# Performance work log

Hardware: AMD Instinct MI355X
Metric: run time of the kernel (lower is better)

Reference implementation:

```python
import jax, jax.numpy as jnp
import numpy as np
import math

B, L, D, H = 2, 2048, 1024, 16

def setup_inputs() -> dict:
    key = jax.random.key(0)
    ks = jax.random.split(key, 5)
    return {
        "query": jax.random.normal(ks[0], (B, L, D), dtype=jnp.float32),
        "key": jax.random.normal(ks[1], (B, L, D), dtype=jnp.float32),
        "value": jax.random.normal(ks[2], (B, L, D), dtype=jnp.float32),
        "w_out": jax.random.normal(ks[3], (D, D), dtype=jnp.float32) * (1.0 / math.sqrt(D)),
        "b_out": jnp.zeros((D,), dtype=jnp.float32),
    }

def reference(query, key, value, w_out, b_out):
    b, l, d_model = query.shape
    num_heads = H
    head_dim = d_model // num_heads
    scaling = 1.0 / math.sqrt(d_model)  # NOTE: module scales by embed_dim, not head_dim

    def reshape(x):
        return x.reshape(b, l, num_heads, head_dim).transpose(0, 2, 1, 3)  # [B,H,L,hd]

    q, k, v = reshape(query), reshape(key), reshape(value)
    scores = jnp.einsum("bhqd,bhkd->bhqk", q, k) * scaling  # [B,H,L,L]

    u = max(1, int(math.ceil(math.log(l + 1))))  # static: 8 for L=2048
    _, topk_idx = jax.lax.top_k(scores, u)  # [B,H,L,u]

    # scatter True at top-u key positions per query
    bi = jnp.arange(b)[:, None, None, None]
    hi = jnp.arange(num_heads)[None, :, None, None]
    qi = jnp.arange(l)[None, None, :, None]
    mask = jnp.zeros(scores.shape, dtype=bool).at[bi, hi, qi, topk_idx].set(True)

    scores_masked = jnp.where(mask, scores, -jnp.inf)
    attn_weights = jax.nn.softmax(scores_masked, axis=-1)  # [B,H,L,L]

    attn_out = jnp.einsum("bhqk,bhkd->bhqd", attn_weights, v)
    attn_out = attn_out.transpose(0, 2, 1, 3).reshape(b, l, d_model)
    attn_out = attn_out @ w_out.T + b_out  # nn.Linear
    return attn_out, attn_weights
```

## Files before the change

### kernel.cpp

```cpp
#include <hip/hip_runtime.h>
#include <math.h>

#define BB 2
#define LL 2048
#define DD 1024
#define HH 16
#define SCALE 0.03125f

#define ATTN_ELEMS ((size_t)BB * LL * DD)

typedef unsigned short u16;
typedef __attribute__((ext_vector_type(8))) short bf16x8;
typedef __attribute__((ext_vector_type(4))) short s16x4;
typedef __attribute__((ext_vector_type(4))) float f32x4;

__device__ __forceinline__ u16 f2bf_rne(float f) {
    union { float f; unsigned u; } c; c.f = f;
    unsigned u = c.u;
    u += 0x7fffu + ((u >> 16) & 1u);
    return (u16)(u >> 16);
}

__device__ __forceinline__ void splitbf(float x, short& h, short& l) {
    union { float f; unsigned u; } c; c.f = x;
    unsigned uh = c.u & 0xFFFF0000u;
    h = (short)(uh >> 16);
    union { unsigned u; float f; } ch; ch.u = uh;
    l = (short)f2bf_rne(x - ch.f);
}

__device__ __forceinline__ void insert8(float (&tv)[8], int (&ti)[8], float cv, int ci) {
    bool g0 = cv > tv[0], g1 = cv > tv[1], g2 = cv > tv[2], g3 = cv > tv[3],
         g4 = cv > tv[4], g5 = cv > tv[5], g6 = cv > tv[6];
    tv[7] = g6 ? tv[6] : cv;                 ti[7] = g6 ? ti[6] : ci;
    tv[6] = g5 ? tv[5] : (g6 ? cv : tv[6]);  ti[6] = g5 ? ti[5] : (g6 ? ci : ti[6]);
    tv[5] = g4 ? tv[4] : (g5 ? cv : tv[5]);  ti[5] = g4 ? ti[4] : (g5 ? ci : ti[5]);
    tv[4] = g3 ? tv[3] : (g4 ? cv : tv[4]);  ti[4] = g3 ? ti[3] : (g4 ? ci : ti[4]);
    tv[3] = g2 ? tv[2] : (g3 ? cv : tv[3]);  ti[3] = g2 ? ti[2] : (g3 ? ci : ti[3]);
    tv[2] = g1 ? tv[1] : (g2 ? cv : tv[2]);  ti[2] = g1 ? ti[1] : (g2 ? ci : ti[2]);
    tv[1] = g0 ? tv[0] : (g1 ? cv : tv[1]);  ti[1] = g0 ? ti[0] : (g1 ? ci : ti[1]);
    tv[0] = g0 ? cv : tv[0];                 ti[0] = g0 ? ci : ti[0];
}

__device__ __forceinline__ void insert12(float (&tv)[12], int (&ti)[12], float cv, int ci) {
    bool g0 = cv > tv[0], g1 = cv > tv[1], g2 = cv > tv[2], g3 = cv > tv[3],
         g4 = cv > tv[4], g5 = cv > tv[5], g6 = cv > tv[6], g7 = cv > tv[7],
         g8 = cv > tv[8], g9 = cv > tv[9], g10 = cv > tv[10];
    tv[11] = g10 ? tv[10] : cv;                 ti[11] = g10 ? ti[10] : ci;
    tv[10] = g9 ? tv[9] : (g10 ? cv : tv[10]);  ti[10] = g9 ? ti[9] : (g10 ? ci : ti[10]);
    tv[9]  = g8 ? tv[8] : (g9 ? cv : tv[9]);    ti[9]  = g8 ? ti[8] : (g9 ? ci : ti[9]);
    tv[8]  = g7 ? tv[7] : (g8 ? cv : tv[8]);    ti[8]  = g7 ? ti[7] : (g8 ? ci : ti[8]);
    tv[7]  = g6 ? tv[6] : (g7 ? cv : tv[7]);    ti[7]  = g6 ? ti[6] : (g7 ? ci : ti[7]);
    tv[6]  = g5 ? tv[5] : (g6 ? cv : tv[6]);    ti[6]  = g5 ? ti[5] : (g6 ? ci : ti[6]);
    tv[5]  = g4 ? tv[4] : (g5 ? cv : tv[5]);    ti[5]  = g4 ? ti[4] : (g5 ? ci : ti[5]);
    tv[4]  = g3 ? tv[3] : (g4 ? cv : tv[4]);    ti[4]  = g3 ? ti[3] : (g4 ? ci : ti[4]);
    tv[3]  = g2 ? tv[2] : (g3 ? cv : tv[3]);    ti[3]  = g2 ? ti[2] : (g3 ? ci : ti[3]);
    tv[2]  = g1 ? tv[1] : (g2 ? cv : tv[2]);    ti[2]  = g1 ? ti[1] : (g2 ? ci : ti[2]);
    tv[1]  = g0 ? tv[0] : (g1 ? cv : tv[1]);    ti[1]  = g0 ? ti[0] : (g1 ? ci : ti[1]);
    tv[0]  = g0 ? cv : tv[0];                   ti[0]  = g0 ? ci : ti[0];
}

__device__ __forceinline__ void merge4(
    const float* v0, const int* i0, const float* v1, const int* i1,
    const float* v2, const int* i2, const float* v3, const int* i3,
    float* ov, int* oi)
{
    int p0 = 0, p1 = 0, p2 = 0, p3 = 0;
    #pragma unroll
    for (int s = 0; s < 8; ++s) {
        float a0 = v0[p0], a1 = v1[p1], a2 = v2[p2], a3 = v3[p3];
        int   b0 = i0[p0], b1 = i1[p1], b2 = i2[p2], b3 = i3[p3];
        float bv = a0; int bi = b0; int bc = 0;
        if (a1 > bv || (a1 == bv && b1 < bi)) { bv = a1; bi = b1; bc = 1; }
        if (a2 > bv || (a2 == bv && b2 < bi)) { bv = a2; bi = b2; bc = 2; }
        if (a3 > bv || (a3 == bv && b3 < bi)) { bv = a3; bi = b3; bc = 3; }
        p0 += (bc == 0); p1 += (bc == 1); p2 += (bc == 2); p3 += (bc == 3);
        ov[s] = bv; oi[s] = bi;
    }
}


__global__ __launch_bounds__(256) void prep_k_kernel(
    const float* __restrict__ k, u16* __restrict__ khi, u16* __restrict__ klo)
{
    int gid = blockIdx.x * 256 + threadIdx.x;
    int li   = gid & 15;
    int qd   = (gid >> 4) & 3;
    int c    = (gid >> 6) & 1;
    int s    = (gid >> 7) & 127;
    int head = gid >> 14;
    int b = head >> 4, h = head & 15;
    const float* src = k + ((size_t)(b * LL + s * 16 + li)) * DD + h * 64 + c * 32 + qd * 8;
    float x[8];
    *(f32x4*)x       = *(const f32x4*)src;
    *(f32x4*)(x + 4) = *(const f32x4*)(src + 4);
    bf16x8 h8, l8;
    #pragma unroll
    for (int e = 0; e < 8; ++e) { short hh, ll; splitbf(x[e], hh, ll); h8[e] = hh; l8[e] = ll; }
    *(bf16x8*)&khi[(size_t)gid * 8] = h8;
    *(bf16x8*)&klo[(size_t)gid * 8] = l8;
}

__global__ __launch_bounds__(256) void prep_w_kernel(
    const float* __restrict__ w, u16* __restrict__ whi, u16* __restrict__ wlo)
{
    int gid = blockIdx.x * 256 + threadIdx.x;
    int li = gid & 15;
    int qd = (gid >> 4) & 3;
    int c  = (gid >> 6) & 3;
    int nt = (gid >> 8) & 3;
    int kc = (gid >> 10) & 7;
    int nb = gid >> 13;
    const float* src = w + (size_t)(nb * 64 + nt * 16 + li) * DD + kc * 128 + c * 32 + qd * 8;
    float x[8];
    *(f32x4*)x       = *(const f32x4*)src;
    *(f32x4*)(x + 4) = *(const f32x4*)(src + 4);
    bf16x8 h8, l8;
    #pragma unroll
    for (int e = 0; e < 8; ++e) { short hh, ll; splitbf(x[e], hh, ll); h8[e] = hh; l8[e] = ll; }
    *(bf16x8*)&whi[(size_t)gid * 8] = h8;
    *(bf16x8*)&wlo[(size_t)gid * 8] = l8;
}

__global__ __launch_bounds__(256) void attn_fast_kernel(
    const float* __restrict__ q, const float* __restrict__ k, const float* __restrict__ v,
    const u16* __restrict__ khi_g, const u16* __restrict__ klo_g,
    float* __restrict__ aw, u16* __restrict__ chi, u16* __restrict__ clo)
{
    const int swz  = (blockIdx.x & 7) * 128 + (blockIdx.x >> 3);
    const int qt   = swz & 31;
    const int h    = (swz >> 5) & 15;
    const int b    = swz >> 9;
    const int t    = threadIdx.x;
    const int wv   = t >> 6;
    const int lane = t & 63;
    const int li   = lane & 15;
    const int quad = lane >> 4;

    __shared__ float dv[64][48];
    __shared__ u16   di_s[64][48];
    __shared__ u16   cidx[64][12];

    f32x4* awz = (f32x4*)(aw + (((size_t)(b * HH + h) * LL) + (size_t)qt * 64) * LL);
    const f32x4 zero4 = {0.f, 0.f, 0.f, 0.f};

    bf16x8 qh0, ql0, qh1, ql1;
    {
        const float* qrow = q + ((size_t)(b * LL + qt * 64 + wv * 16 + li)) * DD + h * 64;
        float x[8];
        *(f32x4*)x       = *(const f32x4*)(qrow + quad * 8);
        *(f32x4*)(x + 4) = *(const f32x4*)(qrow + quad * 8 + 4);
        #pragma unroll
        for (int e = 0; e < 8; ++e) { short hh, ll; splitbf(x[e], hh, ll); qh0[e] = hh; ql0[e] = ll; }
        *(f32x4*)x       = *(const f32x4*)(qrow + 32 + quad * 8);
        *(f32x4*)(x + 4) = *(const f32x4*)(qrow + 32 + quad * 8 + 4);
        #pragma unroll
        for (int e = 0; e < 8; ++e) { short hh, ll; splitbf(x[e], hh, ll); qh1[e] = hh; ql1[e] = ll; }
    }

    float tv[12]; int tix[12];
    #pragma unroll
    for (int s = 0; s < 12; ++s) { tv[s] = -INFINITY; tix[s] = 0; }

    const u16* khb = khi_g + (size_t)(b * HH + h) * 131072 + (size_t)lane * 8;
    const u16* klb = klo_g + (size_t)(b * HH + h) * 131072 + (size_t)lane * 8;

    bf16x8 kh0 = *(const bf16x8*)(khb);
    bf16x8 kh1 = *(const bf16x8*)(khb + 512);
    bf16x8 kl0 = *(const bf16x8*)(klb);
    bf16x8 kl1 = *(const bf16x8*)(klb + 512);

    #pragma unroll 2
    for (int s = 0; s < 128; ++s) {
        const int sn = (s + 1) & 127;
        bf16x8 nh0 = *(const bf16x8*)(khb + (size_t)sn * 1024);
        bf16x8 nh1 = *(const bf16x8*)(khb + (size_t)sn * 1024 + 512);
        bf16x8 nl0 = *(const bf16x8*)(klb + (size_t)sn * 1024);
        bf16x8 nl1 = *(const bf16x8*)(klb + (size_t)sn * 1024 + 512);

        awz[s * 256 + t] = zero4;

        f32x4 c4a = {0.f, 0.f, 0.f, 0.f};
        f32x4 c4b = {0.f, 0.f, 0.f, 0.f};
        c4a = __builtin_amdgcn_mfma_f32_16x16x32_bf16(kh0, qh0, c4a, 0, 0, 0);
        c4b = __builtin_amdgcn_mfma_f32_16x16x32_bf16(kh1, qh1, c4b, 0, 0, 0);
        c4a = __builtin_amdgcn_mfma_f32_16x16x32_bf16(kl0, qh0, c4a, 0, 0, 0);
        c4b = __builtin_amdgcn_mfma_f32_16x16x32_bf16(kl1, qh1, c4b, 0, 0, 0);
        c4a = __builtin_amdgcn_mfma_f32_16x16x32_bf16(kh0, ql0, c4a, 0, 0, 0);
        c4b = __builtin_amdgcn_mfma_f32_16x16x32_bf16(kh1, ql1, c4b, 0, 0, 0);

        const int ci0 = s * 16 + quad * 4;
        #pragma unroll
        for (int r = 0; r < 4; ++r) {
            float cv = (c4a[r] + c4b[r]) * SCALE;
            if (cv > tv[11]) insert12(tv, tix, cv, ci0 + r);
        }
        kh0 = nh0; kh1 = nh1; kl0 = nl0; kl1 = nl1;
    }

    {
        const int row = wv * 16 + li;
        #pragma unroll
        for (int s = 0; s < 12; ++s) {
            dv[row][quad * 12 + s]   = tv[s];
            di_s[row][quad * 12 + s] = (u16)tix[s];
        }
    }
    __syncthreads();

    if (t < 64) {
        const float* v0 = &dv[t][0];   const u16* i0 = &di_s[t][0];
        const float* v1 = &dv[t][12];  const u16* i1 = &di_s[t][12];
        const float* v2 = &dv[t][24];  const u16* i2 = &di_s[t][24];
        const float* v3 = &dv[t][36];  const u16* i3 = &di_s[t][36];
        int p0 = 0, p1 = 0, p2 = 0, p3 = 0;
        #pragma unroll
        for (int s = 0; s < 12; ++s) {
            float a0 = v0[p0], a1 = v1[p1], a2 = v2[p2], a3 = v3[p3];
            int   b0 = i0[p0], b1 = i1[p1], b2 = i2[p2], b3 = i3[p3];
            float bv = a0; int bi = b0; int bc = 0;
            if (a1 > bv || (a1 == bv && b1 < bi)) { bv = a1; bi = b1; bc = 1; }
            if (a2 > bv || (a2 == bv && b2 < bi)) { bv = a2; bi = b2; bc = 2; }
            if (a3 > bv || (a3 == bv && b3 < bi)) { bv = a3; bi = b3; bc = 3; }
            p0 += (bc == 0); p1 += (bc == 1); p2 += (bc == 2); p3 += (bc == 3);
            cidx[t][s] = (u16)bi;
        }
    }
    __syncthreads();

    float* cs = &dv[0][0];
    for (int task = t; task < 768; task += 256) {
        int row = task / 12, c = task - row * 12;
        const float* qp = q + ((size_t)(b * LL + qt * 64 + row)) * DD + h * 64;
        const float* kp = k + ((size_t)(b * LL + (int)cidx[row][c])) * DD + h * 64;
        float acc = 0.f;
        for (int d4 = 0; d4 < 16; ++d4) {
            f32x4 qa = *(const f32x4*)(qp + d4 * 4);
            f32x4 ka = *(const f32x4*)(kp + d4 * 4);
            acc = fmaf(qa[0], ka[0], acc);
            acc = fmaf(qa[1], ka[1], acc);
            acc = fmaf(qa[2], ka[2], acc);
            acc = fmaf(qa[3], ka[3], acc);
        }
        cs[row * 12 + c] = acc * SCALE;
    }
    __syncthreads();

    float* wrow = &dv[0][0] + 1024;
    int*   wix  = (int*)&di_s[0][0];
    if (t < 64) {
        float vv[12]; int ii[12];
        #pragma unroll
        for (int c = 0; c < 12; ++c) { vv[c] = cs[t * 12 + c]; ii[c] = (int)cidx[t][c]; }
        float fv[8]; int fi[8];
        #pragma unroll
        for (int s = 0; s < 8; ++s) {
            float bv = -INFINITY; int bi = 0x7fffffff; int bc = 0;
            #pragma unroll
            for (int c = 0; c < 12; ++c) {
                if (vv[c] > bv || (vv[c] == bv && ii[c] < bi)) { bv = vv[c]; bi = ii[c]; bc = c; }
            }
            vv[bc] = -INFINITY;
            fv[s] = bv; fi[s] = bi;
        }
        float m = fv[0];
        float e0[8]; float sum = 0.f;
        #pragma unroll
        for (int s = 0; s < 8; ++s) { e0[s] = __expf(fv[s] - m); sum += e0[s]; }
        float inv = 1.0f / sum;
        float* awrow = aw + (((size_t)(b * HH + h) * LL) + (size_t)qt * 64 + t) * LL;
        #pragma unroll
        for (int s = 0; s < 8; ++s) {
            float w8 = e0[s] * inv;
            awrow[fi[s]] = w8;
            wrow[t * 8 + s] = w8; wix[t * 8 + s] = fi[s];
        }
    }
    __syncthreads();

    const float* vbase = v + ((size_t)b * LL) * DD + h * 64;
    #pragma unroll
    for (int i = 0; i < 4; ++i) {
        int id = i * 256 + t;
        int row = id >> 4, seg = id & 15;
        f32x4 acc = {0.f, 0.f, 0.f, 0.f};
        #pragma unroll
        for (int s = 0; s < 8; ++s) {
            float ws = wrow[row * 8 + s];
            f32x4 vvv = *(const f32x4*)(vbase + (size_t)wix[row * 8 + s] * DD + seg * 4);
            acc[0] = fmaf(ws, vvv[0], acc[0]);
            acc[1] = fmaf(ws, vvv[1], acc[1]);
            acc[2] = fmaf(ws, vvv[2], acc[2]);
            acc[3] = fmaf(ws, vvv[3], acc[3]);
        }
        size_t off = ((size_t)(b * LL + qt * 64 + row)) * DD + h * 64 + seg * 4;
        s16x4 h4, l4;
        #pragma unroll
        for (int j = 0; j < 4; ++j) { short hh, ll; splitbf(acc[j], hh, ll); h4[j] = hh; l4[j] = ll; }
        *(s16x4*)(chi + off) = h4;
        *(s16x4*)(clo + off) = l4;
    }
}

__global__ __launch_bounds__(256) void linear_fast_kernel(
    const u16* __restrict__ chi, const u16* __restrict__ clo,
    const u16* __restrict__ whi, const u16* __restrict__ wlo,
    const float* __restrict__ bias, float* __restrict__ out)
{
    const int bid  = blockIdx.x;
    const int nb   = bid & 15, mb = bid >> 4;
    const int t    = threadIdx.x;
    const int wv   = t >> 6;
    const int lane = t & 63;
    const int li   = lane & 15;
    const int quad = lane >> 4;

    f32x4 acc0 = {0.f,0.f,0.f,0.f}, acc1 = {0.f,0.f,0.f,0.f},
          acc2 = {0.f,0.f,0.f,0.f}, acc3 = {0.f,0.f,0.f,0.f};

    const u16* ah_row = chi + (size_t)(mb * 64 + wv * 16 + li) * DD + quad * 8;
    const u16* al_row = clo + (size_t)(mb * 64 + wv * 16 + li) * DD + quad * 8;
    const size_t wboff = (size_t)nb * 65536 + (size_t)lane * 8;

    for (int kc = 0; kc < 8; ++kc) {
        const u16* wb_h = whi + wboff + kc * 8192;
        const u16* wb_l = wlo + wboff + kc * 8192;
        #pragma unroll
        for (int c = 0; c < 4; ++c) {
            bf16x8 ah = *(const bf16x8*)(ah_row + kc * 128 + c * 32);
            bf16x8 al = *(const bf16x8*)(al_row + kc * 128 + c * 32);
            bf16x8 bh0 = *(const bf16x8*)(wb_h + c * 512);
            bf16x8 bl0 = *(const bf16x8*)(wb_l + c * 512);
            bf16x8 bh1 = *(const bf16x8*)(wb_h + 2048 + c * 512);
            bf16x8 bl1 = *(const bf16x8*)(wb_l + 2048 + c * 512);
            bf16x8 bh2 = *(const bf16x8*)(wb_h + 4096 + c * 512);
            bf16x8 bl2 = *(const bf16x8*)(wb_l + 4096 + c * 512);
            bf16x8 bh3 = *(const bf16x8*)(wb_h + 6144 + c * 512);
            bf16x8 bl3 = *(const bf16x8*)(wb_l + 6144 + c * 512);
            acc0 = __builtin_amdgcn_mfma_f32_16x16x32_bf16(ah, bh0, acc0, 0, 0, 0);
            acc0 = __builtin_amdgcn_mfma_f32_16x16x32_bf16(ah, bl0, acc0, 0, 0, 0);
            acc0 = __builtin_amdgcn_mfma_f32_16x16x32_bf16(al, bh0, acc0, 0, 0, 0);
            acc1 = __builtin_amdgcn_mfma_f32_16x16x32_bf16(ah, bh1, acc1, 0, 0, 0);
            acc1 = __builtin_amdgcn_mfma_f32_16x16x32_bf16(ah, bl1, acc1, 0, 0, 0);
            acc1 = __builtin_amdgcn_mfma_f32_16x16x32_bf16(al, bh1, acc1, 0, 0, 0);
            acc2 = __builtin_amdgcn_mfma_f32_16x16x32_bf16(ah, bh2, acc2, 0, 0, 0);
            acc2 = __builtin_amdgcn_mfma_f32_16x16x32_bf16(ah, bl2, acc2, 0, 0, 0);
            acc2 = __builtin_amdgcn_mfma_f32_16x16x32_bf16(al, bh2, acc2, 0, 0, 0);
            acc3 = __builtin_amdgcn_mfma_f32_16x16x32_bf16(ah, bh3, acc3, 0, 0, 0);
            acc3 = __builtin_amdgcn_mfma_f32_16x16x32_bf16(ah, bl3, acc3, 0, 0, 0);
            acc3 = __builtin_amdgcn_mfma_f32_16x16x32_bf16(al, bh3, acc3, 0, 0, 0);
        }
    }

    #pragma unroll
    for (int st = 0; st < 4; ++st) {
        f32x4 a = (st == 0) ? acc0 : (st == 1) ? acc1 : (st == 2) ? acc2 : acc3;
        int col = nb * 64 + st * 16 + li;
        float bb2 = bias[col];
        #pragma unroll
        for (int r = 0; r < 4; ++r)
            out[(size_t)(mb * 64 + wv * 16 + quad * 4 + r) * DD + col] = a[r] + bb2;
    }
}


__global__ __launch_bounds__(256) void attn_kernel(
    const float* __restrict__ q, const float* __restrict__ k, const float* __restrict__ v,
    float* __restrict__ aw, float* __restrict__ ctx)
{
    const int bid  = blockIdx.x;
    const int qt   = bid & 31;
    const int h    = (bid >> 5) & 15;
    const int b    = bid >> 9;
    const int t    = threadIdx.x;
    const int wv   = t >> 6;
    const int lane = t & 63;
    const int li   = lane & 15;
    const int quad = lane >> 4;

    __shared__ __align__(16) char smA[32768];
    __shared__ float s2v[32][4][8];
    __shared__ int   s2i[32][4][8];
    __shared__ int   cidx[32][12];
    __shared__ float cs[32][12];
    __shared__ float wrow[64][8];
    __shared__ int   wix[64][8];
    u16* khi = (u16*)smA;
    u16* klo = (u16*)(smA + 16384);

    const float* kbase = k + ((size_t)b * LL) * DD + h * 64;
    f32x4* awz = (f32x4*)(aw + (((size_t)(b * HH + h) * LL) + (size_t)qt * 64) * LL);
    const f32x4 zero4 = {0.f, 0.f, 0.f, 0.f};

    bf16x8 qh0, ql0, qh1, ql1;
    {
        const float* qrow = q + ((size_t)(b * LL + qt * 64 + wv * 16 + li)) * DD + h * 64;
        float x[8];
        *(f32x4*)x       = *(const f32x4*)(qrow + quad * 8);
        *(f32x4*)(x + 4) = *(const f32x4*)(qrow + quad * 8 + 4);
        #pragma unroll
        for (int e = 0; e < 8; ++e) { short hh, ll; splitbf(x[e], hh, ll); qh0[e] = hh; ql0[e] = ll; }
        *(f32x4*)x       = *(const f32x4*)(qrow + 32 + quad * 8);
        *(f32x4*)(x + 4) = *(const f32x4*)(qrow + 32 + quad * 8 + 4);
        #pragma unroll
        for (int e = 0; e < 8; ++e) { short hh, ll; splitbf(x[e], hh, ll); qh1[e] = hh; ql1[e] = ll; }
    }

    float tv[4][8]; int tix[4][8];
    #pragma unroll
    for (int r = 0; r < 4; ++r)
        #pragma unroll
        for (int s = 0; s < 8; ++s) { tv[r][s] = -INFINITY; tix[r][s] = 0; }

    for (int iter = 0; iter < 16; ++iter) {
        __syncthreads();
        #pragma unroll
        for (int j = 0; j < 4; ++j) {
            int f   = j * 256 + t;
            int col = f >> 3;
            int c   = (f >> 2) & 1;
            int qd  = f & 3;
            const float* src = kbase + (size_t)(iter * 128 + col) * DD + c * 32 + qd * 8;
            float x[8];
            *(f32x4*)x       = *(const f32x4*)src;
            *(f32x4*)(x + 4) = *(const f32x4*)(src + 4);
            bf16x8 h8, l8;
            #pragma unroll
            for (int e = 0; e < 8; ++e) { short hh, ll; splitbf(x[e], hh, ll); h8[e] = hh; l8[e] = ll; }
            int off = (((col >> 4) * 2 + c) << 9) + (qd << 7) + ((col & 15) << 3);
            *(bf16x8*)&khi[off] = h8;
            *(bf16x8*)&klo[off] = l8;
        }
        #pragma unroll
        for (int i = 0; i < 8; ++i) awz[iter * 2048 + i * 256 + t] = zero4;
        __syncthreads();

        #pragma unroll
        for (int s = 0; s < 8; ++s) {
            int fo = s << 10;
            bf16x8 kh0 = *(bf16x8*)&khi[fo + (lane << 3)];
            bf16x8 kh1 = *(bf16x8*)&khi[fo + 512 + (lane << 3)];
            bf16x8 kl0 = *(bf16x8*)&klo[fo + (lane << 3)];
            bf16x8 kl1 = *(bf16x8*)&klo[fo + 512 + (lane << 3)];
            f32x4 c4 = {0.f, 0.f, 0.f, 0.f};
            c4 = __builtin_amdgcn_mfma_f32_16x16x32_bf16(qh0, kh0, c4, 0, 0, 0);
            c4 = __builtin_amdgcn_mfma_f32_16x16x32_bf16(qh1, kh1, c4, 0, 0, 0);
            c4 = __builtin_amdgcn_mfma_f32_16x16x32_bf16(qh0, kl0, c4, 0, 0, 0);
            c4 = __builtin_amdgcn_mfma_f32_16x16x32_bf16(qh1, kl1, c4, 0, 0, 0);
            c4 = __builtin_amdgcn_mfma_f32_16x16x32_bf16(ql0, kh0, c4, 0, 0, 0);
            c4 = __builtin_amdgcn_mfma_f32_16x16x32_bf16(ql1, kh1, c4, 0, 0, 0);
            int ci = iter * 128 + s * 16 + li;
            #pragma unroll
            for (int r = 0; r < 4; ++r) {
                float cv = c4[r] * SCALE;
                if (cv > tv[r][7]) insert8(tv[r], tix[r], cv, ci);
            }
        }
    }

    float* mv = (float*)smA;
    int*   mi = (int*)(smA + 16384);
    for (int bb = 0; bb < 2; ++bb) {
        __syncthreads();
        if ((wv >> 1) == bb) {
            int rl0 = (wv & 1) * 16 + quad * 4;
            #pragma unroll
            for (int r = 0; r < 4; ++r) {
                int base = (rl0 + r) * 128 + li * 8;
                #pragma unroll
                for (int s = 0; s < 8; ++s) { mv[base + s] = tv[r][s]; mi[base + s] = tix[r][s]; }
            }
        }
        __syncthreads();
        if (t < 128) {
            int rr = t >> 2, p = t & 3;
            int base = rr * 128 + p * 32;
            merge4(&mv[base], &mi[base], &mv[base + 8], &mi[base + 8],
                   &mv[base + 16], &mi[base + 16], &mv[base + 24], &mi[base + 24],
                   s2v[rr][p], s2i[rr][p]);
        }
        __syncthreads();
        if (t < 32) {
            int rr = t;
            int pp[4] = {0, 0, 0, 0};
            #pragma unroll
            for (int s = 0; s < 12; ++s) {
                float bv = -INFINITY; int bi = 0x7fffffff; int bc = 0;
                #pragma unroll
                for (int l = 0; l < 4; ++l) {
                    if (pp[l] < 8) {
                        float hv = s2v[rr][l][pp[l]]; int hi2 = s2i[rr][l][pp[l]];
                        if (hv > bv || (hv == bv && hi2 < bi)) { bv = hv; bi = hi2; bc = l; }
                    }
                }
                pp[bc] += 1;
                cidx[rr][s] = bi;
            }
        }
        __syncthreads();
        for (int task = t; task < 384; task += 256) {
            int row = task / 12, c = task - row * 12;
            const float* qp = q + ((size_t)(b * LL + qt * 64 + bb * 32 + row)) * DD + h * 64;
            const float* kp = k + ((size_t)(b * LL + cidx[row][c])) * DD + h * 64;
            float acc = 0.f;
            for (int d4 = 0; d4 < 16; ++d4) {
                f32x4 qa = *(const f32x4*)(qp + d4 * 4);
                f32x4 ka = *(const f32x4*)(kp + d4 * 4);
                acc = fmaf(qa[0], ka[0], acc);
                acc = fmaf(qa[1], ka[1], acc);
                acc = fmaf(qa[2], ka[2], acc);
                acc = fmaf(qa[3], ka[3], acc);
            }
            cs[row][c] = acc * SCALE;
        }
        __syncthreads();
        if (t < 32) {
            int rr = t;
            float vv[12]; int ii[12];
            #pragma unroll
            for (int c = 0; c < 12; ++c) { vv[c] = cs[rr][c]; ii[c] = cidx[rr][c]; }
            float fv[8]; int fi[8];
            #pragma unroll
            for (int s = 0; s < 8; ++s) {
                float bv = -INFINITY; int bi = 0x7fffffff; int bc = 0;
                #pragma unroll
                for (int c = 0; c < 12; ++c) {
                    if (vv[c] > bv || (vv[c] == bv && ii[c] < bi)) { bv = vv[c]; bi = ii[c]; bc = c; }
                }
                vv[bc] = -INFINITY;
                fv[s] = bv; fi[s] = bi;
            }
            float m = fv[0];
            float e0[8]; float sum = 0.f;
            #pragma unroll
            for (int s = 0; s < 8; ++s) { e0[s] = __expf(fv[s] - m); sum += e0[s]; }
            float inv = 1.0f / sum;
            int grow = bb * 32 + rr;
            float* awrow = aw + (((size_t)(b * HH + h) * LL) + (size_t)qt * 64 + grow) * LL;
            #pragma unroll
            for (int s = 0; s < 8; ++s) {
                float w8 = e0[s] * inv;
                awrow[fi[s]] = w8;
                wrow[grow][s] = w8; wix[grow][s] = fi[s];
            }
        }
    }
    __syncthreads();

    const float* vbase = v + ((size_t)b * LL) * DD + h * 64;
    #pragma unroll
    for (int i = 0; i < 4; ++i) {
        int id = i * 256 + t;
        int row = id >> 4, seg = id & 15;
        f32x4 acc = {0.f, 0.f, 0.f, 0.f};
        #pragma unroll
        for (int s = 0; s < 8; ++s) {
            float ws = wrow[row][s];
            f32x4 vvv = *(const f32x4*)(vbase + (size_t)wix[row][s] * DD + seg * 4);
            acc[0] = fmaf(ws, vvv[0], acc[0]);
            acc[1] = fmaf(ws, vvv[1], acc[1]);
            acc[2] = fmaf(ws, vvv[2], acc[2]);
            acc[3] = fmaf(ws, vvv[3], acc[3]);
        }
        *(f32x4*)(ctx + ((size_t)(b * LL + qt * 64 + row)) * DD + h * 64 + seg * 4) = acc;
    }
}

__global__ __launch_bounds__(256) void linear_ws_kernel(
    const float* __restrict__ ctx, const float* __restrict__ w,
    const float* __restrict__ bias, float* __restrict__ out)
{
    const int bid  = blockIdx.x;
    const int nb   = bid & 15, mb = bid >> 4;
    const int t    = threadIdx.x;
    const int wv   = t >> 6;
    const int lane = t & 63;
    const int li   = lane & 15;
    const int quad = lane >> 4;

    __shared__ u16 bhi[8192], blo[8192];

    f32x4 acc0 = {0.f,0.f,0.f,0.f}, acc1 = {0.f,0.f,0.f,0.f},
          acc2 = {0.f,0.f,0.f,0.f}, acc3 = {0.f,0.f,0.f,0.f};
    const float* arow = ctx + (size_t)(mb * 64 + wv * 16 + li) * DD;

    for (int kc = 0; kc < 8; ++kc) {
        __syncthreads();
        #pragma unroll
        for (int j = 0; j < 4; ++j) {
            int f   = j * 256 + t;
            int col = f >> 4;
            int c   = (f >> 2) & 3;
            int qd  = f & 3;
            const float* src = w + (size_t)(nb * 64 + col) * DD + kc * 128 + c * 32 + qd * 8;
            float x[8];
            *(f32x4*)x       = *(const f32x4*)src;
            *(f32x4*)(x + 4) = *(const f32x4*)(src + 4);
            bf16x8 h8, l8;
            #pragma unroll
            for (int e = 0; e < 8; ++e) { short hh, ll; splitbf(x[e], hh, ll); h8[e] = hh; l8[e] = ll; }
            int off = (((col >> 4) * 4 + c) << 9) + (qd << 7) + ((col & 15) << 3);
            *(bf16x8*)&bhi[off] = h8;
            *(bf16x8*)&blo[off] = l8;
        }
        __syncthreads();

        bf16x8 ah[4], al[4];
        #pragma unroll
        for (int c = 0; c < 4; ++c) {
            float x[8];
            *(f32x4*)x       = *(const f32x4*)(arow + kc * 128 + c * 32 + quad * 8);
            *(f32x4*)(x + 4) = *(const f32x4*)(arow + kc * 128 + c * 32 + quad * 8 + 4);
            #pragma unroll
            for (int e = 0; e < 8; ++e) { short hh, ll; splitbf(x[e], hh, ll); ah[c][e] = hh; al[c][e] = ll; }
        }
        #pragma unroll
        for (int c = 0; c < 4; ++c) {
            bf16x8 bh0 = *(bf16x8*)&bhi[(( 0 + c) << 9) + (lane << 3)];
            bf16x8 bl0 = *(bf16x8*)&blo[(( 0 + c) << 9) + (lane << 3)];
            bf16x8 bh1 = *(bf16x8*)&bhi[(( 4 + c) << 9) + (lane << 3)];
            bf16x8 bl1 = *(bf16x8*)&blo[(( 4 + c) << 9) + (lane << 3)];
            bf16x8 bh2 = *(bf16x8*)&bhi[(( 8 + c) << 9) + (lane << 3)];
            bf16x8 bl2 = *(bf16x8*)&blo[(( 8 + c) << 9) + (lane << 3)];
            bf16x8 bh3 = *(bf16x8*)&bhi[((12 + c) << 9) + (lane << 3)];
            bf16x8 bl3 = *(bf16x8*)&blo[((12 + c) << 9) + (lane << 3)];
            acc0 = __builtin_amdgcn_mfma_f32_16x16x32_bf16(ah[c], bh0, acc0, 0, 0, 0);
            acc0 = __builtin_amdgcn_mfma_f32_16x16x32_bf16(ah[c], bl0, acc0, 0, 0, 0);
            acc0 = __builtin_amdgcn_mfma_f32_16x16x32_bf16(al[c], bh0, acc0, 0, 0, 0);
            acc1 = __builtin_amdgcn_mfma_f32_16x16x32_bf16(ah[c], bh1, acc1, 0, 0, 0);
            acc1 = __builtin_amdgcn_mfma_f32_16x16x32_bf16(ah[c], bl1, acc1, 0, 0, 0);
            acc1 = __builtin_amdgcn_mfma_f32_16x16x32_bf16(al[c], bh1, acc1, 0, 0, 0);
            acc2 = __builtin_amdgcn_mfma_f32_16x16x32_bf16(ah[c], bh2, acc2, 0, 0, 0);
            acc2 = __builtin_amdgcn_mfma_f32_16x16x32_bf16(ah[c], bl2, acc2, 0, 0, 0);
            acc2 = __builtin_amdgcn_mfma_f32_16x16x32_bf16(al[c], bh2, acc2, 0, 0, 0);
            acc3 = __builtin_amdgcn_mfma_f32_16x16x32_bf16(ah[c], bh3, acc3, 0, 0, 0);
            acc3 = __builtin_amdgcn_mfma_f32_16x16x32_bf16(ah[c], bl3, acc3, 0, 0, 0);
            acc3 = __builtin_amdgcn_mfma_f32_16x16x32_bf16(al[c], bh3, acc3, 0, 0, 0);
        }
    }

    #pragma unroll
    for (int st = 0; st < 4; ++st) {
        f32x4 a = (st == 0) ? acc0 : (st == 1) ? acc1 : (st == 2) ? acc2 : acc3;
        int col = nb * 64 + st * 16 + li;
        float bb2 = bias[col];
        #pragma unroll
        for (int r = 0; r < 4; ++r)
            out[(size_t)(mb * 64 + wv * 16 + quad * 4 + r) * DD + col] = a[r] + bb2;
    }
}

__global__ __launch_bounds__(256) void linear_inplace_kernel(
    float* io, const float* __restrict__ w, const float* __restrict__ bias)
{
    __shared__ u16 ahi[16384], alo[16384];
    const int t    = threadIdx.x;
    const int m0   = blockIdx.x * 16;
    const int wv   = t >> 6;
    const int lane = t & 63;
    const int li   = lane & 15;
    const int quad = lane >> 4;

    #pragma unroll
    for (int i = 0; i < 8; ++i) {
        int id  = i * 256 + t;
        int row = id >> 7;
        int c   = (id >> 2) & 31;
        int qd  = id & 3;
        const float* src = io + (size_t)(m0 + row) * DD + c * 32 + qd * 8;
        float x[8];
        *(f32x4*)x       = *(const f32x4*)src;
        *(f32x4*)(x + 4) = *(const f32x4*)(src + 4);
        bf16x8 h8, l8;
        #pragma unroll
        for (int e = 0; e < 8; ++e) { short hh, ll; splitbf(x[e], hh, ll); h8[e] = hh; l8[e] = ll; }
        int off = (c << 9) + (qd << 7) + (row << 3);
        *(bf16x8*)&ahi[off] = h8;
        *(bf16x8*)&alo[off] = l8;
    }
    __syncthreads();

    f32x4 acc[16];
    #pragma unroll
    for (int i = 0; i < 16; ++i) acc[i] = (f32x4){0.f, 0.f, 0.f, 0.f};

    for (int c = 0; c < 32; ++c) {
        bf16x8 ah = *(bf16x8*)&ahi[(c << 9) + (lane << 3)];
        bf16x8 al = *(bf16x8*)&alo[(c << 9) + (lane << 3)];
        #pragma unroll
        for (int sub = 0; sub < 16; ++sub) {
            int col = wv * 256 + sub * 16 + li;
            const float* src = w + (size_t)col * DD + c * 32 + quad * 8;
            float x[8];
            *(f32x4*)x       = *(const f32x4*)src;
            *(f32x4*)(x + 4) = *(const f32x4*)(src + 4);
            bf16x8 bh, bl;
            #pragma unroll
            for (int e = 0; e < 8; ++e) { short hh, ll; splitbf(x[e], hh, ll); bh[e] = hh; bl[e] = ll; }
            acc[sub] = __builtin_amdgcn_mfma_f32_16x16x32_bf16(ah, bh, acc[sub], 0, 0, 0);
            acc[sub] = __builtin_amdgcn_mfma_f32_16x16x32_bf16(ah, bl, acc[sub], 0, 0, 0);
            acc[sub] = __builtin_amdgcn_mfma_f32_16x16x32_bf16(al, bh, acc[sub], 0, 0, 0);
        }
    }

    #pragma unroll
    for (int sub = 0; sub < 16; ++sub) {
        int col = wv * 256 + sub * 16 + li;
        float bb2 = bias[col];
        #pragma unroll
        for (int r = 0; r < 4; ++r)
            io[(size_t)(m0 + quad * 4 + r) * DD + col] = acc[sub][r] + bb2;
    }
}

extern "C" void kernel_launch(void* const* d_in, const int* in_sizes, int n_in,
                              void* d_out, int out_size, void* d_ws, size_t ws_size,
                              hipStream_t stream) {
    const float* q    = (const float*)d_in[0];
    const float* k    = (const float*)d_in[1];
    const float* v    = (const float*)d_in[2];
    const float* w    = (const float*)d_in[3];
    const float* bias = (const float*)d_in[4];

    float* out = (float*)d_out;
    float* aw  = out + ATTN_ELEMS;

    const size_t CHI_ELE = ATTN_ELEMS;
    const size_t KSP_ELE = 4194304;
    const size_t WSP_ELE = 1048576;
    const size_t need_fast = (2 * CHI_ELE + 2 * KSP_ELE + 2 * WSP_ELE) * sizeof(u16);

    if (d_ws != nullptr && ws_size >= need_fast) {
        u16* chi = (u16*)d_ws;
        u16* clo = chi + CHI_ELE;
        u16* khi = clo + CHI_ELE;
        u16* klo = khi + KSP_ELE;
        u16* whi = klo + KSP_ELE;
        u16* wlo = whi + WSP_ELE;
        prep_k_kernel<<<2048, 256, 0, stream>>>(k, khi, klo);
        prep_w_kernel<<<512, 256, 0, stream>>>(w, whi, wlo);
        attn_fast_kernel<<<BB * HH * (LL / 64), 256, 0, stream>>>(q, k, v, khi, klo, aw, chi, clo);
        linear_fast_kernel<<<(BB * LL / 64) * (DD / 64), 256, 0, stream>>>(chi, clo, whi, wlo, bias, out);
    } else {
        const bool use_ws = (d_ws != nullptr) && (ws_size >= ATTN_ELEMS * sizeof(float));
        float* ctx = use_ws ? (float*)d_ws : out;
        attn_kernel<<<BB * HH * (LL / 64), 256, 0, stream>>>(q, k, v, aw, ctx);
        if (use_ws) {
            linear_ws_kernel<<<(BB * LL / 64) * (DD / 64), 256, 0, stream>>>(ctx, w, bias, out);
        } else {
            linear_inplace_kernel<<<BB * LL / 16, 256, 0, stream>>>(out, w, bias);
        }
    }
}
```

Before: 1.077 ms.

## Select top-12 key groups by group max, then rescore 96 candidates in fp32

The score loop now handles two 16-key tiles per iteration and inserts only the per-thread group maximum over 8 keys into the running top-12 list. This replaces up to four insertions per tile. The fp32 refinement stage then rescores all 96 candidate keys from the 12 selected groups, using per-thread top-8 lists that are merged with tie-breaking. Shared memory is reorganised into a single aliased arena. The design cuts insertion work in the hot loop but makes the exact rescoring pass eight times larger, and correctness now depends on the true top-8 falling inside the top-12 groups.

```diff
diff --git a/kernel.cpp b/kernel.cpp
--- a/kernel.cpp
+++ b/kernel.cpp
@@ -32,6 +32,24 @@
 __device__ __forceinline__ void insert8(float (&tv)[8], int (&ti)[8], float cv, int ci) {
     bool g0 = cv > tv[0], g1 = cv > tv[1], g2 = cv > tv[2], g3 = cv > tv[3],
          g4 = cv > tv[4], g5 = cv > tv[5], g6 = cv > tv[6];
+    tv[7] = g6 ? tv[6] : cv;                 ti[7] = g6 ? ti[6] : ci;
+    tv[6] = g5 ? tv[5] : (g6 ? cv : tv[6]);  ti[6] = g5 ? ti[5] : (g6 ? ci : ti[6]);
+    tv[5] = g4 ? tv[4] : (g5 ? cv : tv[5]);  ti[5] = g4 ? ti[4] : (g5 ? ci : ti[5]);
+    tv[4] = g3 ? tv[3] : (g4 ? cv : tv[4]);  ti[4] = g3 ? ti[3] : (g4 ? ci : ti[4]);
+    tv[3] = g2 ? tv[2] : (g3 ? cv : tv[3]);  ti[3] = g2 ? ti[2] : (g3 ? ci : ti[3]);
+    tv[2] = g1 ? tv[1] : (g2 ? cv : tv[2]);  ti[2] = g1 ? ti[1] : (g2 ? ci : ti[2]);
+    tv[1] = g0 ? tv[0] : (g1 ? cv : tv[1]);  ti[1] = g0 ? ti[0] : (g1 ? ci : ti[1]);
+    tv[0] = g0 ? cv : tv[0];                 ti[0] = g0 ? ci : ti[0];
+}
+
+__device__ __forceinline__ void insert8t(float (&tv)[8], int (&ti)[8], float cv, int ci) {
+    bool g0 = cv > tv[0] || (cv == tv[0] && ci < ti[0]);
+    bool g1 = cv > tv[1] || (cv == tv[1] && ci < ti[1]);
+    bool g2 = cv > tv[2] || (cv == tv[2] && ci < ti[2]);
+    bool g3 = cv > tv[3] || (cv == tv[3] && ci < ti[3]);
+    bool g4 = cv > tv[4] || (cv == tv[4] && ci < ti[4]);
+    bool g5 = cv > tv[5] || (cv == tv[5] && ci < ti[5]);
+    bool g6 = cv > tv[6] || (cv == tv[6] && ci < ti[6]);
     tv[7] = g6 ? tv[6] : cv;                 ti[7] = g6 ? ti[6] : ci;
     tv[6] = g5 ? tv[5] : (g6 ? cv : tv[6]);  ti[6] = g5 ? ti[5] : (g6 ? ci : ti[6]);
     tv[5] = g4 ? tv[4] : (g5 ? cv : tv[5]);  ti[5] = g4 ? ti[4] : (g5 ? ci : ti[5]);
@@ -137,9 +155,14 @@
     const int li   = lane & 15;
     const int quad = lane >> 4;
 
-    __shared__ float dv[64][48];
-    __shared__ u16   di_s[64][48];
-    __shared__ u16   cidx[64][12];
+    __shared__ __align__(16) char arena[19968];
+    u16*   gsel = (u16*)(arena);
+    float* dv   = (float*)(arena + 1536);
+    u16*   dg   = (u16*)(arena + 13824);
+    float* s2v  = (float*)(arena + 1536);
+    u16*   s2i  = (u16*)(arena + 9728);
+    float* wrow = (float*)(arena + 13824);
+    u16*   wixs = (u16*)(arena + 15872);
 
     f32x4* awz = (f32x4*)(aw + (((size_t)(b * HH + h) * LL) + (size_t)qt * 64) * LL);
     const f32x4 zero4 = {0.f, 0.f, 0.f, 0.f};
@@ -158,61 +181,78 @@
         for (int e = 0; e < 8; ++e) { short hh, ll; splitbf(x[e], hh, ll); qh1[e] = hh; ql1[e] = ll; }
     }
 
-    float tv[12]; int tix[12];
-    #pragma unroll
-    for (int s = 0; s < 12; ++s) { tv[s] = -INFINITY; tix[s] = 0; }
+    float tv[12]; int tg[12];
+    #pragma unroll
+    for (int s = 0; s < 12; ++s) { tv[s] = -INFINITY; tg[s] = 0; }
 
     const u16* khb = khi_g + (size_t)(b * HH + h) * 131072 + (size_t)lane * 8;
     const u16* klb = klo_g + (size_t)(b * HH + h) * 131072 + (size_t)lane * 8;
 
-    bf16x8 kh0 = *(const bf16x8*)(khb);
-    bf16x8 kh1 = *(const bf16x8*)(khb + 512);
-    bf16x8 kl0 = *(const bf16x8*)(klb);
-    bf16x8 kl1 = *(const bf16x8*)(klb + 512);
-
-    #pragma unroll 2
-    for (int s = 0; s < 128; ++s) {
-        const int sn = (s + 1) & 127;
-        bf16x8 nh0 = *(const bf16x8*)(khb + (size_t)sn * 1024);
-        bf16x8 nh1 = *(const bf16x8*)(khb + (size_t)sn * 1024 + 512);
-        bf16x8 nl0 = *(const bf16x8*)(klb + (size_t)sn * 1024);
-        bf16x8 nl1 = *(const bf16x8*)(klb + (size_t)sn * 1024 + 512);
-
-        awz[s * 256 + t] = zero4;
-
-        f32x4 c4a = {0.f, 0.f, 0.f, 0.f};
-        f32x4 c4b = {0.f, 0.f, 0.f, 0.f};
-        c4a = __builtin_amdgcn_mfma_f32_16x16x32_bf16(kh0, qh0, c4a, 0, 0, 0);
-        c4b = __builtin_amdgcn_mfma_f32_16x16x32_bf16(kh1, qh1, c4b, 0, 0, 0);
-        c4a = __builtin_amdgcn_mfma_f32_16x16x32_bf16(kl0, qh0, c4a, 0, 0, 0);
-        c4b = __builtin_amdgcn_mfma_f32_16x16x32_bf16(kl1, qh1, c4b, 0, 0, 0);
-        c4a = __builtin_amdgcn_mfma_f32_16x16x32_bf16(kh0, ql0, c4a, 0, 0, 0);
-        c4b = __builtin_amdgcn_mfma_f32_16x16x32_bf16(kh1, ql1, c4b, 0, 0, 0);
-
-        const int ci0 = s * 16 + quad * 4;
-        #pragma unroll
-        for (int r = 0; r < 4; ++r) {
-            float cv = (c4a[r] + c4b[r]) * SCALE;
-            if (cv > tv[11]) insert12(tv, tix, cv, ci0 + r);
-        }
-        kh0 = nh0; kh1 = nh1; kl0 = nl0; kl1 = nl1;
+    bf16x8 Ah0 = *(const bf16x8*)(khb);
+    bf16x8 Ah1 = *(const bf16x8*)(khb + 512);
+    bf16x8 Al0 = *(const bf16x8*)(klb);
+    bf16x8 Al1 = *(const bf16x8*)(klb + 512);
+    bf16x8 Bh0 = *(const bf16x8*)(khb + 1024);
+    bf16x8 Bh1 = *(const bf16x8*)(khb + 1536);
+    bf16x8 Bl0 = *(const bf16x8*)(klb + 1024);
+    bf16x8 Bl1 = *(const bf16x8*)(klb + 1536);
+
+    for (int sp = 0; sp < 64; ++sp) {
+        const int spn = (sp + 1) & 63;
+        const size_t off = (size_t)spn * 2048;
+        bf16x8 NAh0 = *(const bf16x8*)(khb + off);
+        bf16x8 NAh1 = *(const bf16x8*)(khb + off + 512);
+        bf16x8 NAl0 = *(const bf16x8*)(klb + off);
+        bf16x8 NAl1 = *(const bf16x8*)(klb + off + 512);
+        bf16x8 NBh0 = *(const bf16x8*)(khb + off + 1024);
+        bf16x8 NBh1 = *(const bf16x8*)(khb + off + 1536);
+        bf16x8 NBl0 = *(const bf16x8*)(klb + off + 1024);
+        bf16x8 NBl1 = *(const bf16x8*)(klb + off + 1536);
+
+        awz[sp * 512 + t]       = zero4;
+        awz[sp * 512 + 256 + t] = zero4;
+
+        f32x4 c4a = {0,0,0,0}, c4b = {0,0,0,0}, d4a = {0,0,0,0}, d4b = {0,0,0,0};
+        c4a = __builtin_amdgcn_mfma_f32_16x16x32_bf16(Ah0, qh0, c4a, 0, 0, 0);
+        c4b = __builtin_amdgcn_mfma_f32_16x16x32_bf16(Ah1, qh1, c4b, 0, 0, 0);
+        d4a = __builtin_amdgcn_mfma_f32_16x16x32_bf16(Bh0, qh0, d4a, 0, 0, 0);
+        d4b = __builtin_amdgcn_mfma_f32_16x16x32_bf16(Bh1, qh1, d4b, 0, 0, 0);
+        c4a = __builtin_amdgcn_mfma_f32_16x16x32_bf16(Al0, qh0, c4a, 0, 0, 0);
+        c4b = __builtin_amdgcn_mfma_f32_16x16x32_bf16(Al1, qh1, c4b, 0, 0, 0);
+        d4a = __builtin_amdgcn_mfma_f32_16x16x32_bf16(Bl0, qh0, d4a, 0, 0, 0);
+        d4b = __builtin_amdgcn_mfma_f32_16x16x32_bf16(Bl1, qh1, d4b, 0, 0, 0);
+        c4a = __builtin_amdgcn_mfma_f32_16x16x32_bf16(Ah0, ql0, c4a, 0, 0, 0);
+        c4b = __builtin_amdgcn_mfma_f32_16x16x32_bf16(Ah1, ql1, c4b, 0, 0, 0);
+        d4a = __builtin_amdgcn_mfma_f32_16x16x32_bf16(Bh0, ql0, d4a, 0, 0, 0);
+        d4b = __builtin_amdgcn_mfma_f32_16x16x32_bf16(Bh1, ql1, d4b, 0, 0, 0);
+
+        float s0 = c4a[0] + c4b[0], s1 = c4a[1] + c4b[1];
+        float s2 = c4a[2] + c4b[2], s3 = c4a[3] + c4b[3];
+        float s4 = d4a[0] + d4b[0], s5 = d4a[1] + d4b[1];
+        float s6 = d4a[2] + d4b[2], s7 = d4a[3] + d4b[3];
+        float m = fmaxf(fmaxf(fmaxf(s0, s1), fmaxf(s2, s3)),
+                        fmaxf(fmaxf(s4, s5), fmaxf(s6, s7)));
+        if (m > tv[11]) insert12(tv, tg, m, sp * 32 + quad * 4);
+
+        Ah0 = NAh0; Ah1 = NAh1; Al0 = NAl0; Al1 = NAl1;
+        Bh0 = NBh0; Bh1 = NBh1; Bl0 = NBl0; Bl1 = NBl1;
     }
 
     {
         const int row = wv * 16 + li;
         #pragma unroll
         for (int s = 0; s < 12; ++s) {
-            dv[row][quad * 12 + s]   = tv[s];
-            di_s[row][quad * 12 + s] = (u16)tix[s];
+            dv[row * 48 + quad * 12 + s] = tv[s];
+            dg[row * 48 + quad * 12 + s] = (u16)tg[s];
         }
     }
     __syncthreads();
 
     if (t < 64) {
-        const float* v0 = &dv[t][0];   const u16* i0 = &di_s[t][0];
-        const float* v1 = &dv[t][12];  const u16* i1 = &di_s[t][12];
-        const float* v2 = &dv[t][24];  const u16* i2 = &di_s[t][24];
-        const float* v3 = &dv[t][36];  const u16* i3 = &di_s[t][36];
+        const float* v0 = &dv[t * 48];       const u16* i0 = &dg[t * 48];
+        const float* v1 = &dv[t * 48 + 12];  const u16* i1 = &dg[t * 48 + 12];
+        const float* v2 = &dv[t * 48 + 24];  const u16* i2 = &dg[t * 48 + 24];
+        const float* v3 = &dv[t * 48 + 36];  const u16* i3 = &dg[t * 48 + 36];
         int p0 = 0, p1 = 0, p2 = 0, p3 = 0;
         #pragma unroll
         for (int s = 0; s < 12; ++s) {
@@ -223,44 +263,58 @@
             if (a2 > bv || (a2 == bv && b2 < bi)) { bv = a2; bi = b2; bc = 2; }
             if (a3 > bv || (a3 == bv && b3 < bi)) { bv = a3; bi = b3; bc = 3; }
             p0 += (bc == 0); p1 += (bc == 1); p2 += (bc == 2); p3 += (bc == 3);
-            cidx[t][s] = (u16)bi;
+            gsel[t * 12 + s] = (u16)bi;
         }
     }
     __syncthreads();
 
-    float* cs = &dv[0][0];
-    for (int task = t; task < 768; task += 256) {
-        int row = task / 12, c = task - row * 12;
+    {
+        const int row = t >> 2, p = t & 3;
         const float* qp = q + ((size_t)(b * LL + qt * 64 + row)) * DD + h * 64;
-        const float* kp = k + ((size_t)(b * LL + (int)cidx[row][c])) * DD + h * 64;
-        float acc = 0.f;
-        for (int d4 = 0; d4 < 16; ++d4) {
-            f32x4 qa = *(const f32x4*)(qp + d4 * 4);
-            f32x4 ka = *(const f32x4*)(kp + d4 * 4);
-            acc = fmaf(qa[0], ka[0], acc);
-            acc = fmaf(qa[1], ka[1], acc);
-            acc = fmaf(qa[2], ka[2], acc);
-            acc = fmaf(qa[3], ka[3], acc);
-        }
-        cs[row * 12 + c] = acc * SCALE;
+        float tv8[8]; int ti8[8];
+        #pragma unroll
+        for (int s = 0; s < 8; ++s) { tv8[s] = -INFINITY; ti8[s] = 0x7fffffff; }
+        for (int j = p * 24; j < p * 24 + 24; ++j) {
+            int gk = (int)gsel[row * 12 + (j >> 3)];
+            int e  = j & 7;
+            int kidx = gk + ((e >> 2) << 4) + (e & 3);
+            const float* kp = k + ((size_t)(b * LL + kidx)) * DD + h * 64;
+            float a0 = 0.f, a1 = 0.f, a2 = 0.f, a3 = 0.f;
+            for (int d4 = 0; d4 < 16; ++d4) {
+                f32x4 qa = *(const f32x4*)(qp + d4 * 4);
+                f32x4 ka = *(const f32x4*)(kp + d4 * 4);
+                a0 = fmaf(qa[0], ka[0], a0);
+                a1 = fmaf(qa[1], ka[1], a1);
+                a2 = fmaf(qa[2], ka[2], a2);
+                a3 = fmaf(qa[3], ka[3], a3);
+            }
+            float sc = ((a0 + a1) + (a2 + a3)) * SCALE;
+            if (sc > tv8[7] || (sc == tv8[7] && kidx < ti8[7])) insert8t(tv8, ti8, sc, kidx);
+        }
+        #pragma unroll
+        for (int s = 0; s < 8; ++s) {
+            s2v[(row * 4 + p) * 8 + s] = tv8[s];
+            s2i[(row * 4 + p) * 8 + s] = (u16)ti8[s];
+        }
     }
     __syncthreads();
 
-    float* wrow = &dv[0][0] + 1024;
-    int*   wix  = (int*)&di_s[0][0];
     if (t < 64) {
-        float vv[12]; int ii[12];
-        #pragma unroll
-        for (int c = 0; c < 12; ++c) { vv[c] = cs[t * 12 + c]; ii[c] = (int)cidx[t][c]; }
+        const float* v0 = &s2v[(t * 4 + 0) * 8]; const u16* i0 = &s2i[(t * 4 + 0) * 8];
+        const float* v1 = &s2v[(t * 4 + 1) * 8]; const u16* i1 = &s2i[(t * 4 + 1) * 8];
+        const float* v2 = &s2v[(t * 4 + 2) * 8]; const u16* i2 = &s2i[(t * 4 + 2) * 8];
+        const float* v3 = &s2v[(t * 4 + 3) * 8]; const u16* i3 = &s2i[(t * 4 + 3) * 8];
+        int p0 = 0, p1 = 0, p2 = 0, p3 = 0;
         float fv[8]; int fi[8];
         #pragma unroll
         for (int s = 0; s < 8; ++s) {
-            float bv = -INFINITY; int bi = 0x7fffffff; int bc = 0;
-            #pragma unroll
-            for (int c = 0; c < 12; ++c) {
-                if (vv[c] > bv || (vv[c] == bv && ii[c] < bi)) { bv = vv[c]; bi = ii[c]; bc = c; }
-            }
-            vv[bc] = -INFINITY;
+            float a0 = v0[p0], a1 = v1[p1], a2 = v2[p2], a3 = v3[p3];
+            int   b0 = i0[p0], b1 = i1[p1], b2 = i2[p2], b3 = i3[p3];
+            float bv = a0; int bi = b0; int bc = 0;
+            if (a1 > bv || (a1 == bv && b1 < bi)) { bv = a1; bi = b1; bc = 1; }
+            if (a2 > bv || (a2 == bv && b2 < bi)) { bv = a2; bi = b2; bc = 2; }
+            if (a3 > bv || (a3 == bv && b3 < bi)) { bv = a3; bi = b3; bc = 3; }
+            p0 += (bc == 0); p1 += (bc == 1); p2 += (bc == 2); p3 += (bc == 3);
             fv[s] = bv; fi[s] = bi;
         }
         float m = fv[0];
@@ -273,7 +327,7 @@
         for (int s = 0; s < 8; ++s) {
             float w8 = e0[s] * inv;
             awrow[fi[s]] = w8;
-            wrow[t * 8 + s] = w8; wix[t * 8 + s] = fi[s];
+            wrow[t * 8 + s] = w8; wixs[t * 8 + s] = (u16)fi[s];
         }
     }
     __syncthreads();
@@ -287,7 +341,7 @@
         #pragma unroll
         for (int s = 0; s < 8; ++s) {
             float ws = wrow[row * 8 + s];
-            f32x4 vvv = *(const f32x4*)(vbase + (size_t)wix[row * 8 + s] * DD + seg * 4);
+            f32x4 vvv = *(const f32x4*)(vbase + (size_t)wixs[row * 8 + s] * DD + seg * 4);
             acc[0] = fmaf(ws, vvv[0], acc[0]);
             acc[1] = fmaf(ws, vvv[1], acc[1]);
             acc[2] = fmaf(ws, vvv[2], acc[2]);
```

New measurement: 935.1 us. 13.1% less time.
